# Optimization experiments

Measured on AMD Instinct MI355X. Metric: run time of the kernel, lower is better.

## Reference

```python
import jax, jax.numpy as jnp
import numpy as np

N, D_IN, D_OUT = 8192, 256, 128

def setup_inputs() -> dict:
    key = jax.random.key(0)
    kx, kq, kk, kv = jax.random.split(key, 4)
    x = jax.random.normal(kx, (N, D_IN), dtype=jnp.float32)
    # original uses torch.rand (uniform [0,1)) for parameters
    weight_query = jax.random.uniform(kq, (D_IN, D_OUT), dtype=jnp.float32)
    weight_key = jax.random.uniform(kk, (D_IN, D_OUT), dtype=jnp.float32)
    weight_value = jax.random.uniform(kv, (D_IN, D_OUT), dtype=jnp.float32)
    return {"x": x, "weight_query": weight_query, "weight_key": weight_key, "weight_value": weight_value}

def reference(x, weight_query, weight_key, weight_value):
    queries = x @ weight_query            # [N, d_out]
    keys = x @ weight_key                 # [N, d_out]
    values = x @ weight_value             # [N, d_out]
    scale = 1.0 / jnp.sqrt(jnp.asarray(keys.shape[-1], dtype=keys.dtype))
    scores = (queries @ keys.T) * scale   # [N, N] — full score matrix, as in original
    weights = jax.nn.softmax(scores, axis=-1)
    return weights @ values               # [N, d_out]
```

## Files before the change

kernel.cpp:

```cpp
#include <hip/hip_runtime.h>
#include <math.h>


typedef float f32x4 __attribute__((ext_vector_type(4)));
typedef float f32x16 __attribute__((ext_vector_type(16)));
typedef __bf16 bf16x8 __attribute__((ext_vector_type(8)));
typedef unsigned short ushort_t;
typedef ushort_t us4 __attribute__((ext_vector_type(4)));
typedef unsigned u32x2 __attribute__((ext_vector_type(2)));

#define N_TOK 8192
#define NSPLIT 8
#define KVB 32
#define NSTEP2 32

static __device__ __forceinline__ f32x16 mfma32(bf16x8 a, bf16x8 b, f32x16 c) {
  return __builtin_amdgcn_mfma_f32_32x32x16_bf16(a, b, c, 0, 0, 0);
}
static __device__ __forceinline__ void f2split(float f, ushort_t& hi, ushort_t& lo) {
  __bf16 h = (__bf16)f;
  float rem = f - (float)h;
  __bf16 l2 = (__bf16)rem;
  hi = __builtin_bit_cast(ushort_t, h);
  lo = __builtin_bit_cast(ushort_t, l2);
}
static __device__ __forceinline__ void gload16(const void* g, void* l) {
  __builtin_amdgcn_global_load_lds(
      (const __attribute__((address_space(1))) unsigned*)g,
      (__attribute__((address_space(3))) unsigned*)l, 16, 0, 0);
}
static __device__ __forceinline__ unsigned cvtpk(float lo, float hi) {
  unsigned w;
  asm("v_cvt_pk_bf16_f32 %0, %1, %2" : "=v"(w) : "v"(lo), "v"(hi));
  return w;
}

__global__ __launch_bounds__(256) void prep_kernel(
    const float* __restrict__ X, const float* __restrict__ Wq,
    const float* __restrict__ Wk, const float* __restrict__ Wv,
    ushort_t* __restrict__ Xh, ushort_t* __restrict__ Xl,
    ushort_t* __restrict__ WTh, ushort_t* __restrict__ WTl) {
  int gid = blockIdx.x * 256 + threadIdx.x;
  if (gid < 524288) {
    float4 v = reinterpret_cast<const float4*>(X)[gid];
    us4 h, l;
    ushort_t hh, ll;
    f2split(v.x, hh, ll); h[0] = hh; l[0] = ll;
    f2split(v.y, hh, ll); h[1] = hh; l[1] = ll;
    f2split(v.z, hh, ll); h[2] = hh; l[2] = ll;
    f2split(v.w, hh, ll); h[3] = hh; l[3] = ll;
    reinterpret_cast<us4*>(Xh)[gid] = h;
    reinterpret_cast<us4*>(Xl)[gid] = l;
  } else if (gid < 524288 + 98304) {
    int e = gid - 524288;
    int y = e >> 15, r = e & 32767;
    int k = r >> 7, c = r & 127;
    const float* W = (y == 0) ? Wq : (y == 1) ? Wk : Wv;
    ushort_t h, l;
    f2split(W[r], h, l);
    WTh[y * 32768 + c * 256 + k] = h;
    WTl[y * 32768 + c * 256 + k] = l;
  }
}

__global__ __launch_bounds__(256) void proj_kernel(
    const ushort_t* __restrict__ Xh, const ushort_t* __restrict__ Xl,
    const ushort_t* __restrict__ WTh, const ushort_t* __restrict__ WTl,
    ushort_t* __restrict__ Qh, ushort_t* __restrict__ Ql,
    ushort_t* __restrict__ Kh, ushort_t* __restrict__ Kl,
    ushort_t* __restrict__ VTh, ushort_t* __restrict__ VTl) {
  __shared__ __align__(16) char sm[49152];
  const int SXH = 0, SXL = 8192, SWH = 16384, SWL = 32768;
  int t = threadIdx.x, l = t & 63, wid = t >> 6;
  int c32 = l & 31, h = l >> 5;
  int wr = wid >> 1, wc = wid & 1;
  int t0 = blockIdx.x * 64, y = blockIdx.y;
  const ushort_t* WThy = WTh + y * 32768;
  const ushort_t* WTly = WTl + y * 32768;

  f32x16 zero = {};
  f32x16 acc[2];
  acc[0] = zero; acc[1] = zero;

  for (int sl = 0; sl < 4; ++sl) {
    int k0 = sl * 64;
    __syncthreads();
    #pragma unroll
    for (int j = 0; j < 12; ++j) {
      int id = wid * 12 + j;
      const ushort_t* src;
      char* dst;
      if (id < 16) {
        const ushort_t* base = (id < 8) ? Xh : Xl;
        int c_ = id & 7;
        int row = 8 * c_ + (l >> 3);
        int slot = l & 7;
        src = base + (size_t)(t0 + row) * 256 + k0 + ((slot ^ (row & 7)) * 8);
        dst = sm + ((id < 8) ? SXH : SXL) + c_ * 1024 + l * 16;
      } else {
        const ushort_t* base = (id < 32) ? WThy : WTly;
        int c_ = (id - 16) & 15;
        int row = 8 * c_ + (l >> 3);
        int slot = l & 7;
        src = base + (size_t)row * 256 + k0 + ((slot ^ (row & 7)) * 8);
        dst = sm + ((id < 32) ? SWH : SWL) + c_ * 1024 + l * 16;
      }
      gload16(src, dst);
    }
    asm volatile("s_waitcnt vmcnt(0)" ::: "memory");
    __syncthreads();
    #pragma unroll
    for (int ks = 0; ks < 4; ++ks) {
      int ar = 32 * wr + c32;
      int ao = ar * 128 + (((2 * ks + h) ^ (ar & 7)) * 16);
      bf16x8 ah = *(const bf16x8*)(sm + SXH + ao);
      bf16x8 axl = *(const bf16x8*)(sm + SXL + ao);
      #pragma unroll
      for (int ct = 0; ct < 2; ++ct) {
        int bc = 64 * wc + 32 * ct + c32;
        int bo = bc * 128 + (((2 * ks + h) ^ (bc & 7)) * 16);
        bf16x8 bh = *(const bf16x8*)(sm + SWH + bo);
        bf16x8 bl2 = *(const bf16x8*)(sm + SWL + bo);
        acc[ct] = mfma32(ah, bh, acc[ct]);
        acc[ct] = mfma32(ah, bl2, acc[ct]);
        acc[ct] = mfma32(axl, bh, acc[ct]);
      }
    }
  }

  const float QS = 0.12751744f;
  if (y < 2) {
    ushort_t* Hh = y ? Kh : Qh;
    ushort_t* Hl = y ? Kl : Ql;
    #pragma unroll
    for (int ct = 0; ct < 2; ++ct)
      #pragma unroll
      for (int r = 0; r < 16; ++r) {
        float v = acc[ct][r];
        if (y == 0) v *= QS;
        int rt = t0 + 32 * wr + (r & 3) + 8 * (r >> 2) + 4 * h;
        int cc = 64 * wc + 32 * ct + c32;
        ushort_t hh, ll;
        f2split(v, hh, ll);
        Hh[(size_t)rt * 128 + cc] = hh;
        Hl[(size_t)rt * 128 + cc] = ll;
      }
  } else {
    __syncthreads();
    #pragma unroll
    for (int ct = 0; ct < 2; ++ct)
      #pragma unroll
      for (int r = 0; r < 16; ++r) {
        float v = acc[ct][r];
        int rtl = 32 * wr + (r & 3) + 8 * (r >> 2) + 4 * h;
        int cc = 64 * wc + 32 * ct + c32;
        ushort_t hh, ll;
        f2split(v, hh, ll);
        *(ushort_t*)(sm + rtl * 272 + cc * 2) = hh;
        *(ushort_t*)(sm + 17408 + rtl * 272 + cc * 2) = ll;
      }
    __syncthreads();
    int cc = t >> 1, hs = t & 1;
    #pragma unroll
    for (int jj = 0; jj < 4; ++jj) {
      int r0 = hs * 32 + jj * 8;
      us4 a, b, a2, b2;
      #pragma unroll
      for (int e = 0; e < 4; ++e) {
        a[e]  = *(const ushort_t*)(sm + (r0 + e) * 272 + cc * 2);
        b[e]  = *(const ushort_t*)(sm + (r0 + 4 + e) * 272 + cc * 2);
        a2[e] = *(const ushort_t*)(sm + 17408 + (r0 + e) * 272 + cc * 2);
        b2[e] = *(const ushort_t*)(sm + 17408 + (r0 + 4 + e) * 272 + cc * 2);
      }
      *(us4*)(VTh + (size_t)cc * N_TOK + t0 + r0) = a;
      *(us4*)(VTh + (size_t)cc * N_TOK + t0 + r0 + 4) = b;
      *(us4*)(VTl + (size_t)cc * N_TOK + t0 + r0) = a2;
      *(us4*)(VTl + (size_t)cc * N_TOK + t0 + r0 + 4) = b2;
    }
  }
}

__global__ __launch_bounds__(256, 2) void attn_kernel(
    const ushort_t* __restrict__ Qh, const ushort_t* __restrict__ Ql,
    const ushort_t* __restrict__ Kh, const ushort_t* __restrict__ Kl,
    const ushort_t* __restrict__ VTh, const ushort_t* __restrict__ VTl,
    float* __restrict__ Op, float* __restrict__ mp, float* __restrict__ lp) {
  extern __shared__ __align__(16) char sm[];
  int t = threadIdx.x, l = t & 63, wid = t >> 6;
  int c32 = l & 31, h = l >> 5;
  int bid = blockIdx.x;
  int split = bid & 7, qt = bid >> 3;
  int qb = qt * 128, kv0 = split * 1024;
  int q_lane = qb + wid * 32 + c32;

  bf16x8 qfh[8], qfl[8];
  #pragma unroll
  for (int ks = 0; ks < 8; ++ks) {
    qfh[ks] = *(const bf16x8*)(Qh + (size_t)q_lane * 128 + ks * 16 + h * 8);
    qfl[ks] = *(const bf16x8*)(Ql + (size_t)q_lane * 128 + ks * 16 + h * 8);
  }

  const ushort_t* gbase;
  int stepstride;
  int offs[8];
  if (wid < 2) {
    gbase = ((wid == 0) ? Kh : Kl) + (size_t)kv0 * 128;
    stepstride = KVB * 128;
    #pragma unroll
    for (int j = 0; j < 8; ++j) {
      int row = 4 * j + (l >> 4);
      offs[j] = row * 128 + (((l & 15) ^ (row & 15)) * 8);
    }
  } else {
    gbase = ((wid == 2) ? VTh : VTl) + kv0;
    stepstride = KVB;
    #pragma unroll
    for (int j = 0; j < 8; ++j) {
      int d = 16 * j + (l >> 2);
      int g = (l & 3) ^ ((l >> 3) & 3);
      offs[j] = d * N_TOK + 8 * g;
    }
  }
  char* ldsbase = sm + wid * 8192 + l * 16;

  f32x16 zero = {};
  f32x16 od[4];
  #pragma unroll
  for (int dt = 0; dt < 4; ++dt) od[dt] = zero;
  float m = -INFINITY, lsum = 0.f;

  {
    const ushort_t* sb = gbase;
    #pragma unroll
    for (int j = 0; j < 8; ++j) gload16(sb + offs[j], ldsbase + j * 1024);
  }

  for (int s = 0; s < NSTEP2; ++s) {
    int cur = s & 1;
    {
      const ushort_t* sb = gbase + (size_t)((s + 1) & (NSTEP2 - 1)) * stepstride;
      char* db = ldsbase + (cur ^ 1) * 32768;
      #pragma unroll
      for (int j = 0; j < 8; ++j) gload16(sb + offs[j], db + j * 1024);
    }
    asm volatile("s_waitcnt vmcnt(8)" ::: "memory");
    __syncthreads();

    const char* bK = sm + cur * 32768;
    const char* bV = bK + 16384;

    f32x16 sc = zero;
    __builtin_amdgcn_s_setprio(1);
    #pragma unroll
    for (int ks = 0; ks < 8; ++ks) {
      int so = ((2 * ks + h) ^ (c32 & 15)) * 16;
      bf16x8 ah = *(const bf16x8*)(bK + c32 * 256 + so);
      bf16x8 al2 = *(const bf16x8*)(bK + 8192 + c32 * 256 + so);
      sc = mfma32(ah, qfh[ks], sc);
      sc = mfma32(ah, qfl[ks], sc);
      sc = mfma32(al2, qfh[ks], sc);
    }
    __builtin_amdgcn_s_setprio(0);

    float pm = sc[0];
    #pragma unroll
    for (int r = 1; r < 16; ++r) pm = fmaxf(pm, sc[r]);
    pm = fmaxf(pm, __shfl_xor(pm, 32));
    if (!__all(pm <= m + 8.0f)) {
      float mn = fmaxf(m, pm);
      float al = exp2f(m - mn);
      m = mn;
      lsum *= al;
      #pragma unroll
      for (int dt = 0; dt < 4; ++dt) od[dt] *= al;
    }
    float ps = 0.f;
    #pragma unroll
    for (int r = 0; r < 16; ++r) { sc[r] = exp2f(sc[r] - m); ps += sc[r]; }
    lsum += ps;

    bf16x8 pf[2];
    #pragma unroll
    for (int ks = 0; ks < 2; ++ks) {
      int r0 = 8 * ks;
      unsigned A0 = cvtpk(sc[r0 + 0], sc[r0 + 1]);
      unsigned A1 = cvtpk(sc[r0 + 2], sc[r0 + 3]);
      unsigned B0 = cvtpk(sc[r0 + 4], sc[r0 + 5]);
      unsigned B1 = cvtpk(sc[r0 + 6], sc[r0 + 7]);
      u32x2 s0 = __builtin_amdgcn_permlane32_swap(A0, B0, false, false);
      u32x2 s1 = __builtin_amdgcn_permlane32_swap(A1, B1, false, false);
      union { unsigned u[4]; bf16x8 v; } cvt;
      cvt.u[0] = s0[0]; cvt.u[1] = s1[0]; cvt.u[2] = s0[1]; cvt.u[3] = s1[1];
      pf[ks] = cvt.v;
    }

    __builtin_amdgcn_s_setprio(1);
    #pragma unroll
    for (int ks = 0; ks < 2; ++ks) {
      #pragma unroll
      for (int dt = 0; dt < 4; ++dt) {
        int row = 32 * dt + c32;
        int so2 = row * 64 + (((2 * ks + h) ^ ((row >> 1) & 3)) * 16);
        bf16x8 vh = *(const bf16x8*)(bV + so2);
        bf16x8 vl2 = *(const bf16x8*)(bV + 8192 + so2);
        od[dt] = mfma32(vh, pf[ks], od[dt]);
        od[dt] = mfma32(vl2, pf[ks], od[dt]);
      }
    }
    __builtin_amdgcn_s_setprio(0);
    __syncthreads();
  }

  lsum += __shfl_xor(lsum, 32);
  #pragma unroll
  for (int dt = 0; dt < 4; ++dt)
    #pragma unroll
    for (int r = 0; r < 16; ++r) {
      int d = 32 * dt + (r & 3) + 8 * (r >> 2) + 4 * h;
      Op[(size_t)(split * 128 + d) * N_TOK + q_lane] = od[dt][r];
    }
  if (h == 0) {
    mp[split * N_TOK + q_lane] = m;
    lp[split * N_TOK + q_lane] = lsum;
  }
}

__global__ __launch_bounds__(256) void merge_kernel(
    const float* __restrict__ Op, const float* __restrict__ mp,
    const float* __restrict__ lp, float* __restrict__ out) {
  __shared__ float accs[32][129];
  __shared__ float Ls[32];
  int t = threadIdx.x;
  int q0 = blockIdx.x * 32;
  int ql = t & 31, dr = t >> 5;
  float mm[NSPLIT], ll[NSPLIT];
  #pragma unroll
  for (int s2 = 0; s2 < NSPLIT; ++s2) {
    mm[s2] = mp[s2 * N_TOK + q0 + ql];
    ll[s2] = lp[s2 * N_TOK + q0 + ql];
  }
  float M = mm[0];
  #pragma unroll
  for (int s2 = 1; s2 < NSPLIT; ++s2) M = fmaxf(M, mm[s2]);
  float w[NSPLIT], L = 0.f;
  #pragma unroll
  for (int s2 = 0; s2 < NSPLIT; ++s2) { w[s2] = exp2f(mm[s2] - M); L += w[s2] * ll[s2]; }
  if (dr == 0) Ls[ql] = L;
  for (int dd = dr; dd < 128; dd += 8) {
    float a = 0.f;
    #pragma unroll
    for (int s2 = 0; s2 < NSPLIT; ++s2)
      a += w[s2] * Op[(size_t)(s2 * 128 + dd) * N_TOK + q0 + ql];
    accs[ql][dd] = a;
  }
  __syncthreads();
  int q = t >> 3, db = (t & 7) * 16;
  float inv = 1.0f / Ls[q];
  #pragma unroll
  for (int jj = 0; jj < 4; ++jj) {
    f32x4 v;
    #pragma unroll
    for (int e = 0; e < 4; ++e) v[e] = accs[q][db + jj * 4 + e] * inv;
    *reinterpret_cast<f32x4*>(out + (size_t)(q0 + q) * 128 + db + jj * 4) = v;
  }
}

extern "C" void kernel_launch(void* const* d_in, const int* in_sizes, int n_in,
                              void* d_out, int out_size, void* d_ws, size_t ws_size,
                              hipStream_t stream) {
  (void)in_sizes; (void)n_in; (void)out_size; (void)ws_size;
  const float* X  = (const float*)d_in[0];
  const float* Wq = (const float*)d_in[1];
  const float* Wk = (const float*)d_in[2];
  const float* Wv = (const float*)d_in[3];
  float* out = (float*)d_out;
  char* ws = (char*)d_ws;

  const size_t MB = 1048576;
  ushort_t* Qh  = (ushort_t*)(ws + 0 * MB);
  ushort_t* Ql  = (ushort_t*)(ws + 2 * MB);
  ushort_t* Kh  = (ushort_t*)(ws + 4 * MB);
  ushort_t* Kl  = (ushort_t*)(ws + 6 * MB);
  ushort_t* VTh = (ushort_t*)(ws + 8 * MB);
  ushort_t* VTl = (ushort_t*)(ws + 10 * MB);
  float* mpp = (float*)(ws + 12 * MB);
  float* lpp = (float*)(ws + 12 * MB + 262144);
  float* Op  = (float*)(ws + 12 * MB + 524288);
  ushort_t* Xh  = (ushort_t*)(ws + 12 * MB + 524288);
  ushort_t* Xl  = (ushort_t*)(ws + 16 * MB + 524288);
  ushort_t* WTh = (ushort_t*)(ws + 20 * MB + 524288);
  ushort_t* WTl = (ushort_t*)(ws + 20 * MB + 524288 + 196608);

  (void)hipFuncSetAttribute((const void*)attn_kernel,
                            hipFuncAttributeMaxDynamicSharedMemorySize, 65536);

  prep_kernel<<<2432, 256, 0, stream>>>(X, Wq, Wk, Wv, Xh, Xl, WTh, WTl);
  proj_kernel<<<dim3(128, 3), 256, 0, stream>>>(Xh, Xl, WTh, WTl,
                                                Qh, Ql, Kh, Kl, VTh, VTl);
  attn_kernel<<<512, 256, 65536, stream>>>(Qh, Ql, Kh, Kl, VTh, VTl, Op, mpp, lpp);
  merge_kernel<<<256, 256, 0, stream>>>(Op, mpp, lpp, out);
}
```

Before: 174.7 us.

## Double KV splits, single-buffer LDS for higher occupancy, store partial outputs in fp16

```diff
diff --git a/kernel.cpp b/kernel.cpp
--- a/kernel.cpp
+++ b/kernel.cpp
@@ -10,9 +10,9 @@
 typedef unsigned u32x2 __attribute__((ext_vector_type(2)));
 
 #define N_TOK 8192
-#define NSPLIT 8
+#define NSPLIT 16
 #define KVB 32
-#define NSTEP2 32
+#define NSTEP3 16
 
 static __device__ __forceinline__ f32x16 mfma32(bf16x8 a, bf16x8 b, f32x16 c) {
   return __builtin_amdgcn_mfma_f32_32x32x16_bf16(a, b, c, 0, 0, 0);
@@ -180,17 +180,17 @@
   }
 }
 
-__global__ __launch_bounds__(256, 2) void attn_kernel(
+__global__ __launch_bounds__(256, 4) void attn_kernel(
     const ushort_t* __restrict__ Qh, const ushort_t* __restrict__ Ql,
     const ushort_t* __restrict__ Kh, const ushort_t* __restrict__ Kl,
     const ushort_t* __restrict__ VTh, const ushort_t* __restrict__ VTl,
-    float* __restrict__ Op, float* __restrict__ mp, float* __restrict__ lp) {
+    _Float16* __restrict__ Op, float* __restrict__ mp, float* __restrict__ lp) {
   extern __shared__ __align__(16) char sm[];
   int t = threadIdx.x, l = t & 63, wid = t >> 6;
   int c32 = l & 31, h = l >> 5;
   int bid = blockIdx.x;
-  int split = bid & 7, qt = bid >> 3;
-  int qb = qt * 128, kv0 = split * 1024;
+  int split = bid & 15, qt = bid >> 4;
+  int qb = qt * 128, kv0 = split * 512;
   int q_lane = qb + wid * 32 + c32;
 
   bf16x8 qfh[8], qfl[8];
@@ -229,25 +229,15 @@
   for (int dt = 0; dt < 4; ++dt) od[dt] = zero;
   float m = -INFINITY, lsum = 0.f;
 
-  {
-    const ushort_t* sb = gbase;
-    #pragma unroll
-    for (int j = 0; j < 8; ++j) gload16(sb + offs[j], ldsbase + j * 1024);
-  }
-
-  for (int s = 0; s < NSTEP2; ++s) {
-    int cur = s & 1;
-    {
-      const ushort_t* sb = gbase + (size_t)((s + 1) & (NSTEP2 - 1)) * stepstride;
-      char* db = ldsbase + (cur ^ 1) * 32768;
-      #pragma unroll
-      for (int j = 0; j < 8; ++j) gload16(sb + offs[j], db + j * 1024);
-    }
-    asm volatile("s_waitcnt vmcnt(8)" ::: "memory");
-    __syncthreads();
-
-    const char* bK = sm + cur * 32768;
-    const char* bV = bK + 16384;
+  #pragma unroll
+  for (int j = 0; j < 8; ++j) gload16(gbase + offs[j], ldsbase + j * 1024);
+
+  for (int s = 0; s < NSTEP3; ++s) {
+    asm volatile("s_waitcnt vmcnt(0)" ::: "memory");
+    __syncthreads();
+
+    const char* bK = sm;
+    const char* bV = sm + 16384;
 
     f32x16 sc = zero;
     __builtin_amdgcn_s_setprio(1);
@@ -309,6 +299,11 @@
     }
     __builtin_amdgcn_s_setprio(0);
     __syncthreads();
+    if (s + 1 < NSTEP3) {
+      const ushort_t* sb = gbase + (size_t)(s + 1) * stepstride;
+      #pragma unroll
+      for (int j = 0; j < 8; ++j) gload16(sb + offs[j], ldsbase + j * 1024);
+    }
   }
 
   lsum += __shfl_xor(lsum, 32);
@@ -317,7 +312,7 @@
     #pragma unroll
     for (int r = 0; r < 16; ++r) {
       int d = 32 * dt + (r & 3) + 8 * (r >> 2) + 4 * h;
-      Op[(size_t)(split * 128 + d) * N_TOK + q_lane] = od[dt][r];
+      Op[(size_t)(split * 128 + d) * N_TOK + q_lane] = (_Float16)od[dt][r];
     }
   if (h == 0) {
     mp[split * N_TOK + q_lane] = m;
@@ -326,7 +321,7 @@
 }
 
 __global__ __launch_bounds__(256) void merge_kernel(
-    const float* __restrict__ Op, const float* __restrict__ mp,
+    const _Float16* __restrict__ Op, const float* __restrict__ mp,
     const float* __restrict__ lp, float* __restrict__ out) {
   __shared__ float accs[32][129];
   __shared__ float Ls[32];
@@ -350,7 +345,7 @@
     float a = 0.f;
     #pragma unroll
     for (int s2 = 0; s2 < NSPLIT; ++s2)
-      a += w[s2] * Op[(size_t)(s2 * 128 + dd) * N_TOK + q0 + ql];
+      a += w[s2] * (float)Op[(size_t)(s2 * 128 + dd) * N_TOK + q0 + ql];
     accs[ql][dd] = a;
   }
   __syncthreads();
@@ -384,19 +379,19 @@
   ushort_t* VTh = (ushort_t*)(ws + 8 * MB);
   ushort_t* VTl = (ushort_t*)(ws + 10 * MB);
   float* mpp = (float*)(ws + 12 * MB);
-  float* lpp = (float*)(ws + 12 * MB + 262144);
-  float* Op  = (float*)(ws + 12 * MB + 524288);
-  ushort_t* Xh  = (ushort_t*)(ws + 12 * MB + 524288);
-  ushort_t* Xl  = (ushort_t*)(ws + 16 * MB + 524288);
-  ushort_t* WTh = (ushort_t*)(ws + 20 * MB + 524288);
-  ushort_t* WTl = (ushort_t*)(ws + 20 * MB + 524288 + 196608);
+  float* lpp = (float*)(ws + 12 * MB + 524288);
+  _Float16* Oph = (_Float16*)(ws + 13 * MB);
+  ushort_t* Xh  = (ushort_t*)(ws + 13 * MB);
+  ushort_t* Xl  = (ushort_t*)(ws + 17 * MB);
+  ushort_t* WTh = (ushort_t*)(ws + 21 * MB);
+  ushort_t* WTl = (ushort_t*)(ws + 21 * MB + 196608);
 
   (void)hipFuncSetAttribute((const void*)attn_kernel,
-                            hipFuncAttributeMaxDynamicSharedMemorySize, 65536);
+                            hipFuncAttributeMaxDynamicSharedMemorySize, 32768);
 
   prep_kernel<<<2432, 256, 0, stream>>>(X, Wq, Wk, Wv, Xh, Xl, WTh, WTl);
   proj_kernel<<<dim3(128, 3), 256, 0, stream>>>(Xh, Xl, WTh, WTl,
                                                 Qh, Ql, Kh, Kl, VTh, VTl);
-  attn_kernel<<<512, 256, 65536, stream>>>(Qh, Ql, Kh, Kl, VTh, VTl, Op, mpp, lpp);
-  merge_kernel<<<256, 256, 0, stream>>>(Op, mpp, lpp, out);
-}
+  attn_kernel<<<1024, 256, 32768, stream>>>(Qh, Ql, Kh, Kl, VTh, VTl, Oph, mpp, lpp);
+  merge_kernel<<<256, 256, 0, stream>>>(Oph, mpp, lpp, out);
+}
```

After: 269.4 us. +54.2%, slower.
